# Optimization experiments

Hardware: AMD Instinct MI355X
Metric: run time of the kernel (lower is better)

Reference implementation:

```python
import jax, jax.numpy as jnp
import numpy as np

OBS_DIM = 115
ID_LO, ID_HI = 97, 108  # one-hot agent-id slice


def setup_inputs() -> dict:
    key = jax.random.key(0)
    k1, k2 = jax.random.split(key)
    a, b, n_agents = 128, 512, 11
    state_dim = n_agents * OBS_DIM  # 1265
    agents_q = jax.random.normal(k1, (a, b, n_agents), dtype=jnp.float32)
    global_state = jax.random.normal(k2, (a, b, state_dim), dtype=jnp.float32)
    return {"agents_q": agents_q, "global_state": global_state}


def reference(agents_q, global_state):
    a, b, n_agents = agents_q.shape
    q = agents_q.reshape(-1, n_agents)                 # [B, A]
    gs = global_state.reshape(-1, global_state.shape[-1])  # [B, A*115]
    B = q.shape[0]

    ball_pos = gs[:, 88:90]                            # [B, 2]
    holder_info = gs[:, 94:97]
    is_my_team = holder_info[:, 1] != 0                # .bool() semantics
    goal = jnp.array([1.0, 0.0], dtype=q.dtype)
    ball_goal_dist = jnp.sqrt(jnp.sum((ball_pos - goal) ** 2, axis=1))
    valid_advance = is_my_team & (ball_goal_dist > 0.19) & (ball_goal_dist < 0.99)

    # all agent obs blocks at once: [B, A, 115]
    obs = gs[:, : n_agents * OBS_DIM].reshape(B, n_agents, OBS_DIM)
    agent_id = jnp.argmax(obs[:, :, ID_LO:ID_HI], axis=-1)        # [B, A] in [0,10]
    pos_x = jnp.take_along_axis(obs, (2 * agent_id)[..., None], axis=-1)[..., 0]
    pos_y = jnp.take_along_axis(obs, (2 * agent_id + 1)[..., None], axis=-1)[..., 0]

    # distance of each agent to ball and to goal: [B, A]
    dist_matrix = jnp.sqrt((pos_x - ball_pos[:, 0:1]) ** 2 + (pos_y - ball_pos[:, 1:2]) ** 2)
    goal_dist_matrix = jnp.sqrt((pos_x - 1.0) ** 2 + pos_y ** 2)

    holder_mask = jax.nn.one_hot(jnp.argmin(dist_matrix, axis=1), n_agents, dtype=q.dtype)
    advance_component = holder_mask * valid_advance[:, None].astype(q.dtype) * 5.0
    position_component = 1.0 / (goal_dist_matrix + 1e-6)
    combined = jnp.where(valid_advance[:, None], advance_component, position_component)

    weights = jax.nn.softmax(combined, axis=1)
    global_q = jnp.sum(q * weights, axis=1, keepdims=True)        # [B, 1]
    return (global_q * n_agents).reshape(a, b, 1)
```

## Files before the change

### kernel.cpp

```cpp
#include <hip/hip_runtime.h>
#include <math.h>

#define OBS_DIM 115
#define N_AGENTS 11
#define ROW_F (N_AGENTS * OBS_DIM)
#define WAVES_PER_BLOCK 4
#define ROWS_PER_WAVE 4
#define ROWS_PER_BLOCK (WAVES_PER_BLOCK * ROWS_PER_WAVE)
#define SLICE_F 388
#define WAVE_F (ROWS_PER_WAVE * SLICE_F)


typedef const __attribute__((address_space(1))) unsigned int gu32;
typedef __attribute__((address_space(3))) unsigned int lu32;

__global__ __launch_bounds__(256) void qmix_kernel(
    const float* __restrict__ q,
    const float* __restrict__ gs,
    float* __restrict__ out,
    int B)
{
    __shared__ float lds[WAVES_PER_BLOCK * WAVE_F];

    const int tid  = threadIdx.x;
    const int wv   = tid >> 6;
    const int lane = tid & 63;
    const int rbase = blockIdx.x * ROWS_PER_BLOCK + wv * ROWS_PER_WAVE;

    int off[6], isq[6];
    #pragma unroll
    for (int p6 = 0; p6 < 6; ++p6) {
        const int mm = p6 * 64 + lane;
        int o = 0, iq = 0;
        if (mm < 242)      { const int a = mm / 22; o = a * OBS_DIM + (mm - a * 22); }
        else if (mm < 363) { const int t = mm - 242; const int a = t / 11;
                             o = a * OBS_DIM + 97 + (t - a * 11); }
        else if (mm == 363) o = 88;
        else if (mm == 364) o = 89;
        else if (mm == 365) o = 95;
        else if (mm < 377) { o = mm - 366; iq = 1; }
        else               o = 0;
        off[p6] = o; isq[p6] = iq;
    }

    #pragma unroll
    for (int p = 0; p < ROWS_PER_WAVE * 6; ++p) {
        const int rl = p / 6;
        const int p6 = p % 6;
        int rr = rbase + rl;
        if (rr >= B) rr = B - 1;
        const float* gbase = isq[p6] ? (q + (size_t)rr * N_AGENTS)
                                     : (gs + (size_t)rr * ROW_F);
        const float* src = gbase + off[p6];
        __builtin_amdgcn_global_load_lds(
            (gu32*)src,
            (lu32*)&lds[wv * WAVE_F + rl * SLICE_F + p6 * 64],
            4, 0, 0);
    }

    __syncthreads();

    const int g  = lane >> 4;
    const int s  = lane & 15;
    const int rr = rbase + g;
    const float* S = &lds[wv * WAVE_F + g * SLICE_F];

    const float bx = S[363], by = S[364], team = S[365];
    const float g0  = bx - 1.0f;
    const float bgd = sqrtf(g0 * g0 + by * by);
    const bool valid = (team != 0.0f) && (bgd > 0.19f) && (bgd < 0.99f);

    float dist = INFINITY;
    float comb = -INFINITY;
    float qv = 0.0f, gd = 0.0f;

    if (s < N_AGENTS) {
        const float* idb = S + 242 + s * 11;
        float best = idb[0]; int bi = 0;
        #pragma unroll
        for (int j = 1; j < 11; ++j) {
            float v = idb[j];
            if (v > best) { best = v; bi = j; }
        }
        const float px = S[s * 22 + 2 * bi];
        const float py = S[s * 22 + 2 * bi + 1];
        const float dx = px - bx, dy = py - by;
        dist = sqrtf(dx * dx + dy * dy);
        const float gx = px - 1.0f;
        gd = sqrtf(gx * gx + py * py);
        qv = S[366 + s];
    }

    int idx = s;
    float d = dist;
    #pragma unroll
    for (int o = 8; o >= 1; o >>= 1) {
        float d2 = __shfl_xor(d, o, 16);
        int   i2 = __shfl_xor(idx, o, 16);
        if (d2 < d || (d2 == d && i2 < idx)) { d = d2; idx = i2; }
    }

    if (s < N_AGENTS)
        comb = valid ? ((s == idx) ? 5.0f : 0.0f)
                     : 1.0f / (gd + 1e-6f);

    float m = comb;
    #pragma unroll
    for (int o = 8; o >= 1; o >>= 1)
        m = fmaxf(m, __shfl_xor(m, o, 16));

    float wgt = expf(comb - m);
    float wq  = wgt * qv;
    #pragma unroll
    for (int o = 8; o >= 1; o >>= 1) {
        wgt += __shfl_xor(wgt, o, 16);
        wq  += __shfl_xor(wq,  o, 16);
    }

    if (s == 0 && rr < B)
        out[rr] = wq * (float)N_AGENTS / wgt;
}

extern "C" void kernel_launch(void* const* d_in, const int* in_sizes, int n_in,
                              void* d_out, int out_size, void* d_ws, size_t ws_size,
                              hipStream_t stream) {
    const float* q  = (const float*)d_in[0];
    const float* gs = (const float*)d_in[1];
    float* out = (float*)d_out;

    int B = in_sizes[0] / N_AGENTS;
    int grid = (B + ROWS_PER_BLOCK - 1) / ROWS_PER_BLOCK;
    qmix_kernel<<<grid, 256, 0, stream>>>(q, gs, out, B);
}
```

Before: 409.5 us.

## Stream full rows into LDS with 16-byte async loads instead of scalar gathers

Replaces the per-element 4-byte gather of the 377 needed values per row with whole-row 16-byte global_load_lds copies, aligned by shifting the row start. q is now read directly from global memory, and the block barrier becomes a per-wave vmcnt wait. This reduces load instruction count and improves coalescing, at the cost of a much larger LDS footprint that may reduce occupancy.

```diff
diff --git a/kernel.cpp b/kernel.cpp
--- a/kernel.cpp
+++ b/kernel.cpp
@@ -3,13 +3,11 @@
 
 #define OBS_DIM 115
 #define N_AGENTS 11
-#define ROW_F (N_AGENTS * OBS_DIM)
+#define ROW_F 1265
+#define ROWS_PER_WAVE 4
 #define WAVES_PER_BLOCK 4
-#define ROWS_PER_WAVE 4
-#define ROWS_PER_BLOCK (WAVES_PER_BLOCK * ROWS_PER_WAVE)
-#define SLICE_F 388
-#define WAVE_F (ROWS_PER_WAVE * SLICE_F)
-
+#define ROWS_PER_BLOCK (ROWS_PER_WAVE * WAVES_PER_BLOCK)
+#define SLICE_F 1280
 
 typedef const __attribute__((address_space(1))) unsigned int gu32;
 typedef __attribute__((address_space(3))) unsigned int lu32;
@@ -20,75 +18,68 @@
     float* __restrict__ out,
     int B)
 {
-    __shared__ float lds[WAVES_PER_BLOCK * WAVE_F];
+    __shared__ float lds[ROWS_PER_BLOCK * SLICE_F];
 
     const int tid  = threadIdx.x;
     const int wv   = tid >> 6;
     const int lane = tid & 63;
     const int rbase = blockIdx.x * ROWS_PER_BLOCK + wv * ROWS_PER_WAVE;
 
-    int off[6], isq[6];
     #pragma unroll
-    for (int p6 = 0; p6 < 6; ++p6) {
-        const int mm = p6 * 64 + lane;
-        int o = 0, iq = 0;
-        if (mm < 242)      { const int a = mm / 22; o = a * OBS_DIM + (mm - a * 22); }
-        else if (mm < 363) { const int t = mm - 242; const int a = t / 11;
-                             o = a * OBS_DIM + 97 + (t - a * 11); }
-        else if (mm == 363) o = 88;
-        else if (mm == 364) o = 89;
-        else if (mm == 365) o = 95;
-        else if (mm < 377) { o = mm - 366; iq = 1; }
-        else               o = 0;
-        off[p6] = o; isq[p6] = iq;
-    }
-
-    #pragma unroll
-    for (int p = 0; p < ROWS_PER_WAVE * 6; ++p) {
-        const int rl = p / 6;
-        const int p6 = p % 6;
+    for (int rl = 0; rl < ROWS_PER_WAVE; ++rl) {
         int rr = rbase + rl;
         if (rr >= B) rr = B - 1;
-        const float* gbase = isq[p6] ? (q + (size_t)rr * N_AGENTS)
-                                     : (gs + (size_t)rr * ROW_F);
-        const float* src = gbase + off[p6];
-        __builtin_amdgcn_global_load_lds(
-            (gu32*)src,
-            (lu32*)&lds[wv * WAVE_F + rl * SLICE_F + p6 * 64],
-            4, 0, 0);
+        const int shift = rr & 3;
+        const float* src = gs + ((size_t)rr * ROW_F - shift);
+        float* dst = &lds[(wv * ROWS_PER_WAVE + rl) * SLICE_F];
+        #pragma unroll
+        for (int p = 0; p < 5; ++p) {
+            const bool active = !(p == 4 && rr == B - 1 && lane >= 60);
+            if (active) {
+                __builtin_amdgcn_global_load_lds(
+                    (gu32*)(src + p * 256 + lane * 4),
+                    (lu32*)(dst + p * 256),
+                    16, 0, 0);
+            }
+        }
     }
-
-    __syncthreads();
 
     const int g  = lane >> 4;
     const int s  = lane & 15;
-    const int rr = rbase + g;
-    const float* S = &lds[wv * WAVE_F + g * SLICE_F];
+    int rr = rbase + g;
+    const bool row_ok = (rr < B);
+    if (!row_ok) rr = B - 1;
 
-    const float bx = S[363], by = S[364], team = S[365];
+    float qv = 0.0f;
+    if (s < N_AGENTS) qv = q[(size_t)rr * N_AGENTS + s];
+
+    asm volatile("s_waitcnt vmcnt(0)" ::: "memory");
+
+    const float* S = &lds[(wv * ROWS_PER_WAVE + g) * SLICE_F + (rr & 3)];
+
+    const float bx = S[88], by = S[89], team = S[95];
     const float g0  = bx - 1.0f;
     const float bgd = sqrtf(g0 * g0 + by * by);
     const bool valid = (team != 0.0f) && (bgd > 0.19f) && (bgd < 0.99f);
 
     float dist = INFINITY;
     float comb = -INFINITY;
-    float qv = 0.0f, gd = 0.0f;
+    float gd = 0.0f;
 
     if (s < N_AGENTS) {
-        const float* idb = S + 242 + s * 11;
+        const float* idb = S + s * OBS_DIM + 97;
         float best = idb[0]; int bi = 0;
         #pragma unroll
         for (int j = 1; j < 11; ++j) {
             float v = idb[j];
             if (v > best) { best = v; bi = j; }
         }
-        const float px = S[s * 22 + 2 * bi];
-        const float py = S[s * 22 + 2 * bi + 1];
+        const float px = S[s * OBS_DIM + 2 * bi];
+        const float py = S[s * OBS_DIM + 2 * bi + 1];
         const float dx = px - bx, dy = py - by;
         dist = sqrtf(dx * dx + dy * dy);
         const float gx = px - 1.0f;
         gd = sqrtf(gx * gx + py * py);
-        qv = S[366 + s];
     }
 
     int idx = s;
@@ -109,16 +100,16 @@
     for (int o = 8; o >= 1; o >>= 1)
         m = fmaxf(m, __shfl_xor(m, o, 16));
 
-    float wgt = expf(comb - m);
-    float wq  = wgt * qv;
+    float w  = expf(comb - m);
+    float wq = w * qv;
     #pragma unroll
     for (int o = 8; o >= 1; o >>= 1) {
-        wgt += __shfl_xor(wgt, o, 16);
-        wq  += __shfl_xor(wq,  o, 16);
+        w  += __shfl_xor(w,  o, 16);
+        wq += __shfl_xor(wq, o, 16);
     }
 
-    if (s == 0 && rr < B)
-        out[rr] = wq * (float)N_AGENTS / wgt;
+    if (s == 0 && row_ok)
+        out[rr] = wq * (float)N_AGENTS / w;
 }
 
 extern "C" void kernel_launch(void* const* d_in, const int* in_sizes, int n_in,
```

Result: slower. 432.9 us (+5.7%).
